# Performance work log

Measured on AMD Instinct MI355X. Metric: run time of the kernel, lower is better.

## Reference

```python
import jax, jax.numpy as jnp
import numpy as np
from jax import lax

GS = 29          # grid_size
DW = 15          # displacement_width
DR = 0.4         # disp_range
N = GS ** 3      # 24389 control points
P = DW ** 2      # 225 in-plane displacements
WIN = (1, 1, 3, 3, 1)
ONE = (1, 1, 1, 1, 1)


def _axis(n):
    # align_corners=False pixel-center coords in [-1, 1], as torch affine_grid
    return (2.0 * jnp.arange(n, dtype=jnp.float32) + 1.0) / n - 1.0


def make_grids():
    a = _axis(GS)
    zc, yc, xc = jnp.meshgrid(a, a, a, indexing='ij')
    grid_xyz = jnp.stack([xc, yc, zc], -1).reshape(-1, 3)  # (N,3) xyz, d-major flatten
    s = DR * _axis(DW)
    A, B = jnp.meshgrid(s, s, indexing='ij')
    Z = jnp.zeros_like(A)
    sx = jnp.stack([B, A, Z], -1).reshape(-1, 3)  # z=0 plane: (s[w], s[h], 0)
    sy = jnp.stack([B, Z, A], -1).reshape(-1, 3)  # y=0 plane: (s[w], 0, s[d])
    sz = jnp.stack([Z, B, A], -1).reshape(-1, 3)  # x=0 plane: (0, s[h], s[d])
    shift_2d = jnp.stack([sx, sy, sz], axis=1)    # (P,3,3): [disp, plane, xyz]
    return grid_xyz, shift_2d


def trilerp(vol, coords, border):
    # vol (C,D,H,W); coords (...,3) normalized xyz; align_corners=False trilinear
    C, D, H, W = vol.shape
    vflat = vol.reshape(C, -1)
    x, y, z = coords[..., 0], coords[..., 1], coords[..., 2]
    ix = 0.5 * ((x + 1.0) * W - 1.0)
    iy = 0.5 * ((y + 1.0) * H - 1.0)
    iz = 0.5 * ((z + 1.0) * D - 1.0)
    x0 = jnp.floor(ix); y0 = jnp.floor(iy); z0 = jnp.floor(iz)
    fx, fy, fz = ix - x0, iy - y0, iz - z0
    x0 = x0.astype(jnp.int32); y0 = y0.astype(jnp.int32); z0 = z0.astype(jnp.int32)
    out = 0.0
    for dz in (0, 1):
        wz = fz if dz else 1.0 - fz
        zi = z0 + dz
        for dy in (0, 1):
            wy = fy if dy else 1.0 - fy
            yi = y0 + dy
            for dx in (0, 1):
                wx = fx if dx else 1.0 - fx
                xi = x0 + dx
                w = wx * wy * wz
                xc = jnp.clip(xi, 0, W - 1)
                yc = jnp.clip(yi, 0, H - 1)
                zc = jnp.clip(zi, 0, D - 1)
                if not border:  # padding_mode='zeros'
                    inb = ((xi >= 0) & (xi < W) & (yi >= 0) & (yi < H) & (zi >= 0) & (zi < D))
                    w = w * inb.astype(vol.dtype)
                idx = (zc * H + yc) * W + xc
                out = out + vflat[:, idx] * w
    return out  # (C, *coords.shape[:-1])


def pad_dh(x):
    # ReplicationPad3d((0,0,2,2,2,2)) on a 5D tensor: pad dims 2 and 3 by 2
    return jnp.pad(x, ((0, 0), (0, 0), (2, 2), (2, 2), (0, 0)), mode='edge')


def minpool(x):
    # -MaxPool3d((3,3,1))(-x)
    return -lax.reduce_window(-x, -jnp.inf, lax.max, WIN, ONE, 'VALID')


def avgpool(x):
    # AvgPool3d((3,3,1), stride=1)
    return lax.reduce_window(x, 0.0, lax.add, WIN, ONE, 'VALID') / 9.0


def grid_smooth(cost):
    # (1,N,DW,DW,3) -> two 3x3 avg passes over the 29^3 control grid (d,h axes)
    cp = cost.transpose(2, 3, 4, 0, 1).reshape(1, 3 * P, GS, GS, GS)
    cp = avgpool(avgpool(pad_dh(cp)))
    return cp.transpose(0, 2, 3, 4, 1).reshape(1, N, DW, DW, 3)


def setup_inputs() -> dict:
    key = jax.random.key(0)
    k1, k2 = jax.random.split(key)
    C, V = 8, 64
    feat00 = jax.random.normal(k1, (1, C, V, V, V), jnp.float32)
    feat50 = jax.random.normal(k2, (1, C, V, V, V), jnp.float32)
    grid_xyz, shift_2d = make_grids()
    shift_2d_min = jnp.array(jnp.broadcast_to(shift_2d[None, None], (1, N, P, 3, 3)))
    alpha = jnp.array([1.0, 0.1, 1.0, 1.0, 0.1, 5.0], jnp.float32)
    return {"feat00": feat00, "feat50": feat50, "shift_2d_min": shift_2d_min,
            "grid_xyz": grid_xyz, "shift_2d": shift_2d, "alpha": alpha}


def reference(feat00, feat50, shift_2d_min, grid_xyz, shift_2d, alpha):
    grid29 = grid_xyz.reshape(GS, GS * GS, 3)
    sm = shift_2d_min.reshape(GS, GS * GS, P, 3, 3)
    f00, f50 = feat00[0], feat50[0]

    def chunk(args):
        g, s = args                                                # (841,3), (841,P,3,3)
        mov = trilerp(f50, g[:, None, None, :] + s, border=True)   # (C,841,P,3)
        fix = trilerp(f00, g, border=False)                        # (C,841)
        ssd = jnp.sum((fix[:, :, None, None] - mov) ** 2, axis=0)  # (841,P,3)
        return alpha[1] + alpha[0] * ssd

    pdd = lax.map(chunk, (grid29, sm)).reshape(1, N, DW, DW, 3)
    cost = avgpool(minpool(pad_dh(pdd)))
    cost = alpha[4] + alpha[2] * pdd + alpha[3] * grid_smooth(cost)
    cost = avgpool(minpool(pad_dh(cost)))
    cost_avg = grid_smooth(cost).reshape(N, P, 3)
    cost_soft = jax.nn.softmax(-alpha[5] * cost_avg, axis=1)
    pred_xyz = 0.5 * jnp.einsum('npk,pkd->nd', cost_soft, shift_2d)
    return cost_soft.reshape(N, 1, DW, DW, 3), pred_xyz, cost_avg
```

## Files before the change

### kernel.cpp

```cpp
#include <hip/hip_runtime.h>
#include <math.h>

#define GS   29
#define GS2  841
#define NCP  24389
#define DW   15
#define PP   225
#define CH   675
#define CHP  676
#define CC   8
#define VV   64
#define V3   262144

typedef __attribute__((ext_vector_type(8))) _Float16 half8;
typedef __attribute__((ext_vector_type(4))) _Float16 half4;

__device__ __forceinline__ float sv(int i) {
    return 0.4f * ((2.f * i + 1.f) * (1.f / 15.f) - 1.f);
}

__global__ __launch_bounds__(256) void make_vols(const float* __restrict__ in,
                                                 _Float16* __restrict__ volA,
                                                 _Float16* __restrict__ volB) {
    int v = blockIdx.x * 256 + threadIdx.x;
    if (v >= V3) return;
    int z = v >> 12, y = (v >> 6) & 63, x = v & 63;
    half8 h;
#pragma unroll
    for (int c = 0; c < CC; c++) h[c] = (_Float16)in[c * V3 + v];
    *(half8*)(volA + (size_t)v * 8) = h;
    *(half8*)(volB + (size_t)((((z << 6) | x) << 6) | y) * 8) = h;
}

__global__ __launch_bounds__(256) void pdd_pool_n(const float* __restrict__ f00,
                                                  const _Float16* __restrict__ volA,
                                                  const _Float16* __restrict__ volB,
                                                  const float* __restrict__ grid,
                                                  const float* __restrict__ alpha,
                                                  _Float16* __restrict__ pdd,
                                                  _Float16* __restrict__ pool) {
    int n = blockIdx.x;
    int tid = threadIdx.x;
    __shared__ __align__(16) _Float16 fixh[8];
    __shared__ float rowp[CH];
    __shared__ float smin[3 * 289];

    float gx = grid[n * 3 + 0], gy = grid[n * 3 + 1], gz = grid[n * 3 + 2];

    if (tid < 8) {
        float ix = 0.5f * ((gx + 1.f) * VV - 1.f);
        float iy = 0.5f * ((gy + 1.f) * VV - 1.f);
        float iz = 0.5f * ((gz + 1.f) * VV - 1.f);
        float x0f = floorf(ix), y0f = floorf(iy), z0f = floorf(iz);
        float fx = ix - x0f, fy = iy - y0f, fz = iz - z0f;
        int x0 = (int)x0f, y0 = (int)y0f, z0 = (int)z0f;
        const float* fc = f00 + tid * V3;
        float acc = 0.f;
        for (int dz = 0; dz < 2; dz++) {
            int zi = z0 + dz; float wz = dz ? fz : 1.f - fz;
            for (int dy = 0; dy < 2; dy++) {
                int yi = y0 + dy; float wy = dy ? fy : 1.f - fy;
                for (int dx = 0; dx < 2; dx++) {
                    int xi = x0 + dx; float wx = dx ? fx : 1.f - fx;
                    if (xi >= 0 && xi < VV && yi >= 0 && yi < VV && zi >= 0 && zi < VV)
                        acc += wx * wy * wz * fc[(zi * VV + yi) * VV + xi];
                }
            }
        }
        fixh[tid] = (_Float16)acc;
    }
    __syncthreads();

    if (tid < PP) {
        int p = tid;
        int h_ = p / 15, w_ = p - 15 * h_;
        float A = sv(h_), B = sv(w_);
        half8 f8 = *(const half8*)fixh;
        float a0 = alpha[0], a1 = alpha[1];

        for (int k = 0; k < 3; k++) {
            float pu, pv, pw;
            const _Float16* vol;
            if (k == 0)      { pu = gx + B; pv = gy + A; pw = gz;     vol = volA; }
            else if (k == 1) { pu = gx + B; pv = gy;     pw = gz + A; vol = volA; }
            else             { pu = gy + B; pv = gx;     pw = gz + A; vol = volB; }

            float iu = 0.5f * ((pu + 1.f) * VV - 1.f);
            float iv = 0.5f * ((pv + 1.f) * VV - 1.f);
            float iw = 0.5f * ((pw + 1.f) * VV - 1.f);
            float u0f = floorf(iu), v0f = floorf(iv), w0f = floorf(iw);
            float fu = iu - u0f, fv = iv - v0f, fw = iw - w0f;
            int u0 = (int)u0f, v0 = (int)v0f, w0 = (int)w0f;

            int p0 = min(max(u0, 0), VV - 2);
            float wAu = (u0 < 0) ? 1.f : ((u0 >= VV - 1) ? 0.f : (1.f - fu));
            float wBu = 1.f - wAu;
            int v0c = min(max(v0, 0), VV - 1), v1c = min(max(v0 + 1, 0), VV - 1);
            int w0c = min(max(w0, 0), VV - 1), w1c = min(max(w0 + 1, 0), VV - 1);
            float wv0 = 1.f - fv, wv1 = fv;
            float ww0 = 1.f - fw, ww1 = fw;

            half8 acc = {0, 0, 0, 0, 0, 0, 0, 0};
#define PAIR(WC, VC, WGT) {                                               \
                float fA_ = (WGT) * wAu, fB_ = (WGT) * wBu;               \
                _Float16 hA_ = (_Float16)fA_, hB_ = (_Float16)fB_;        \
                half8 hA8 = {hA_, hA_, hA_, hA_, hA_, hA_, hA_, hA_};     \
                half8 hB8 = {hB_, hB_, hB_, hB_, hB_, hB_, hB_, hB_};     \
                const _Float16* vp = vol + (size_t)((((WC) * VV) + (VC)) * VV + p0) * 8; \
                half8 lo = *(const half8*)vp;                             \
                half8 hi = *(const half8*)(vp + 8);                       \
                acc += hA8 * lo;                                          \
                acc += hB8 * hi;                                          \
            }
            PAIR(w0c, v0c, ww0 * wv0)
            PAIR(w0c, v1c, ww0 * wv1)
            PAIR(w1c, v0c, ww1 * wv0)
            PAIR(w1c, v1c, ww1 * wv1)
#undef PAIR

            half8 d8 = f8 - acc;
            float ssd = 0.f;
#pragma unroll
            for (int c = 0; c < 8; c++) { float dc = (float)d8[c]; ssd = fmaf(dc, dc, ssd); }
            rowp[p * 3 + k] = a1 + a0 * ssd;
        }
    }
    __syncthreads();

    for (int idx = tid; idx < 867; idx += 256) {
        int k = idx / 289; int r = idx - 289 * k; int a = r / 17; int b = r - 17 * a;
        float mn = 1e30f;
        for (int u = 0; u < 3; u++) {
            int hh = min(max(a + u - 2, 0), 14);
            for (int v = 0; v < 3; v++) {
                int ww = min(max(b + v - 2, 0), 14);
                mn = fminf(mn, rowp[(hh * 15 + ww) * 3 + k]);
            }
        }
        smin[idx] = mn;
    }
    __syncthreads();

    for (int i = tid; i < CH; i += 256) {
        pdd[(size_t)n * CHP + i] = (_Float16)rowp[i];
        int p = i / 3, k = i - 3 * p;
        int h = p / 15, w = p - 15 * h;
        float acc = 0.f;
        for (int a = 0; a < 3; a++)
            for (int b = 0; b < 3; b++)
                acc += smin[k * 289 + (h + a) * 17 + (w + b)];
        pool[(size_t)n * CHP + i] = (_Float16)(acc * (1.f / 9.f));
    }
}

__global__ __launch_bounds__(256) void gs_z4(const _Float16* __restrict__ in,
                                             _Float16* __restrict__ out) {
    const int COLS = GS2 * 169;
    int id = blockIdx.x * 256 + threadIdx.x;
    if (id >= COLS) return;
    int row = id / 169, c4 = id - 169 * row;
    size_t base = (size_t)row * CHP + c4 * 4;
    const size_t ZS = (size_t)GS2 * CHP;
    const float w0 = 1.f / 9.f, w1 = 2.f / 9.f, w2 = 3.f / 9.f;

    half4 h0 = *(const half4*)(in + base);
    half4 h3 = *(const half4*)(in + base + ZS);
    half4 h4 = *(const half4*)(in + base + 2 * ZS);
    float v0[4], v1[4], v2[4], v3[4], v4[4];
#pragma unroll
    for (int j = 0; j < 4; j++) {
        v0[j] = (float)h0[j]; v1[j] = v0[j]; v2[j] = v0[j];
        v3[j] = (float)h3[j]; v4[j] = (float)h4[j];
    }
    for (int z = 0; z < GS; z++) {
        half4 o;
#pragma unroll
        for (int j = 0; j < 4; j++)
            o[j] = (_Float16)(w0 * (v0[j] + v4[j]) + w1 * (v1[j] + v3[j]) + w2 * v2[j]);
        *(half4*)(out + base + (size_t)z * ZS) = o;
        int zn = z + 3; if (zn > GS - 1) zn = GS - 1;
        half4 hn = *(const half4*)(in + base + (size_t)zn * ZS);
#pragma unroll
        for (int j = 0; j < 4; j++) {
            v0[j] = v1[j]; v1[j] = v2[j]; v2[j] = v3[j]; v3[j] = v4[j];
            v4[j] = (float)hn[j];
        }
    }
}

__global__ __launch_bounds__(256) void cost_pool2_y(const _Float16* __restrict__ zs,
                                                    const _Float16* __restrict__ pdd,
                                                    const float* __restrict__ alpha,
                                                    _Float16* __restrict__ pool2) {
    int n = blockIdx.x, tid = threadIdx.x;
    int x = n % GS; int zy = n / GS; int y = zy % GS; int z = zy / GS;
    __shared__ float rowp[CHP];
    __shared__ float smn[17 * 17 * 3];

    if (tid < 169) {
        int c0 = tid * 4;
        float s0 = 0.f, s1 = 0.f, s2 = 0.f, s3 = 0.f;
#pragma unroll
        for (int dy = 0; dy < 5; dy++) {
            int yy = min(max(y + dy - 2, 0), GS - 1);
            size_t off = ((size_t)(z * GS + yy) * GS + x) * CHP + c0;
            float w = (3.f - fabsf((float)dy - 2.f)) * (1.f / 9.f);
            half4 hv = *(const half4*)(zs + off);
            s0 = fmaf(w, (float)hv[0], s0);
            s1 = fmaf(w, (float)hv[1], s1);
            s2 = fmaf(w, (float)hv[2], s2);
            s3 = fmaf(w, (float)hv[3], s3);
        }
        float a2 = alpha[2], a3 = alpha[3], a4 = alpha[4];
        half4 pv = *(const half4*)(pdd + (size_t)n * CHP + c0);
        rowp[c0 + 0] = a4 + a2 * (float)pv[0] + a3 * s0;
        rowp[c0 + 1] = a4 + a2 * (float)pv[1] + a3 * s1;
        rowp[c0 + 2] = a4 + a2 * (float)pv[2] + a3 * s2;
        rowp[c0 + 3] = a4 + a2 * (float)pv[3] + a3 * s3;
    }
    __syncthreads();

    for (int idx = tid; idx < 867; idx += 256) {
        int k = idx / 289; int r = idx - 289 * k; int a = r / 17; int b = r - 17 * a;
        float mn = 1e30f;
        for (int u = 0; u < 3; u++) {
            int hh = min(max(a + u - 2, 0), 14);
            for (int v = 0; v < 3; v++) {
                int ww = min(max(b + v - 2, 0), 14);
                mn = fminf(mn, rowp[(hh * 15 + ww) * 3 + k]);
            }
        }
        smn[idx] = mn;
    }
    __syncthreads();

    for (int i = tid; i < CH; i += 256) {
        int p = i / 3, k = i - 3 * p;
        int h = p / 15, w = p - 15 * h;
        float acc = 0.f;
        for (int a = 0; a < 3; a++)
            for (int b = 0; b < 3; b++)
                acc += smn[k * 289 + (h + a) * 17 + (w + b)];
        pool2[(size_t)n * CHP + i] = (_Float16)(acc * (1.f / 9.f));
    }
}

__global__ __launch_bounds__(256) void smooth_y_softmax(const _Float16* __restrict__ zs,
                                                        const float* __restrict__ alpha,
                                                        float* __restrict__ ca,
                                                        float* __restrict__ soft,
                                                        float* __restrict__ pred) {
    int n = blockIdx.x, tid = threadIdx.x;
    int x = n % GS; int zy = n / GS; int y = zy % GS; int z = zy / GS;
    int wave = tid >> 6, lane = tid & 63;
    __shared__ float vals[CHP];
    __shared__ float partial[3][3];

    if (tid < 169) {
        int c0 = tid * 4;
        float s0 = 0.f, s1 = 0.f, s2 = 0.f, s3 = 0.f;
#pragma unroll
        for (int dy = 0; dy < 5; dy++) {
            int yy = min(max(y + dy - 2, 0), GS - 1);
            size_t off = ((size_t)(z * GS + yy) * GS + x) * CHP + c0;
            float w = (3.f - fabsf((float)dy - 2.f)) * (1.f / 9.f);
            half4 hv = *(const half4*)(zs + off);
            s0 = fmaf(w, (float)hv[0], s0);
            s1 = fmaf(w, (float)hv[1], s1);
            s2 = fmaf(w, (float)hv[2], s2);
            s3 = fmaf(w, (float)hv[3], s3);
        }
        vals[c0 + 0] = s0;
        vals[c0 + 1] = s1;
        vals[c0 + 2] = s2;
        vals[c0 + 3] = s3;
    }
    __syncthreads();

    for (int i = tid; i < CH; i += 256) ca[(size_t)n * CH + i] = vals[i];
    __syncthreads();

    float a5 = alpha[5];
    if (wave < 3) {
        int k = wave;
        float v[4], e[4];
        float m = -1e30f;
#pragma unroll
        for (int j = 0; j < 4; j++) {
            int p = lane + 64 * j;
            v[j] = (p < PP) ? -a5 * vals[p * 3 + k] : -1e30f;
            m = fmaxf(m, v[j]);
        }
#pragma unroll
        for (int o = 32; o > 0; o >>= 1) m = fmaxf(m, __shfl_xor(m, o));
        float sum = 0.f;
#pragma unroll
        for (int j = 0; j < 4; j++) {
            int p = lane + 64 * j;
            e[j] = (p < PP) ? __expf(v[j] - m) : 0.f;
            sum += e[j];
        }
#pragma unroll
        for (int o = 32; o > 0; o >>= 1) sum += __shfl_xor(sum, o);
        float inv = 1.f / sum;
        float px = 0.f, py = 0.f, pz = 0.f;
#pragma unroll
        for (int j = 0; j < 4; j++) {
            int p = lane + 64 * j;
            if (p < PP) {
                float s = e[j] * inv;
                vals[p * 3 + k] = s;
                int h_ = p / 15, w_ = p - 15 * h_;
                float A = sv(h_), B = sv(w_);
                if (k == 0)      { px += s * B; py += s * A; }
                else if (k == 1) { px += s * B; pz += s * A; }
                else             { py += s * B; pz += s * A; }
            }
        }
#pragma unroll
        for (int o = 32; o > 0; o >>= 1) {
            px += __shfl_xor(px, o);
            py += __shfl_xor(py, o);
            pz += __shfl_xor(pz, o);
        }
        if (lane == 0) { partial[k][0] = px; partial[k][1] = py; partial[k][2] = pz; }
    }
    __syncthreads();
    if (tid < 3) pred[(size_t)n * 3 + tid] = 0.5f * (partial[0][tid] + partial[1][tid] + partial[2][tid]);
    for (int i = tid; i < CH; i += 256) soft[(size_t)n * CH + i] = vals[i];
}

extern "C" void kernel_launch(void* const* d_in, const int* in_sizes, int n_in,
                              void* d_out, int out_size, void* d_ws, size_t ws_size,
                              hipStream_t stream) {
    const float* f00   = (const float*)d_in[0];
    const float* f50   = (const float*)d_in[1];
    const float* grid  = (const float*)d_in[3];
    const float* alpha = (const float*)d_in[5];

    float* out0 = (float*)d_out;
    float* out1 = out0 + (size_t)NCP * CH;
    float* out2 = out1 + (size_t)NCP * 3;

    char* ws = (char*)d_ws;
    _Float16* volA = (_Float16*)ws;
    _Float16* volB = volA + (size_t)V3 * 8;
    _Float16* H0 = volB + (size_t)V3 * 8;
    _Float16* H1 = H0 + (size_t)NCP * CHP;
    _Float16* H2 = H1 + (size_t)NCP * CHP;

    make_vols<<<(V3 + 255) / 256, 256, 0, stream>>>(f50, volA, volB);

    pdd_pool_n<<<NCP, 256, 0, stream>>>(f00, volA, volB, grid, alpha, H0, H1);

    const int COLS = GS2 * 169;
    const int gbz = (COLS + 255) / 256;

    gs_z4<<<gbz, 256, 0, stream>>>(H1, H2);
    cost_pool2_y<<<NCP, 256, 0, stream>>>(H2, H0, alpha, H1);

    gs_z4<<<gbz, 256, 0, stream>>>(H1, H2);
    smooth_y_softmax<<<NCP, 256, 0, stream>>>(H2, alpha, out2, out0, out1);
}
```

Measured before the change: 534.2 us.

## Separate min/avg pooling into row/column passes and share per-axis trilinear setup

The 3x3 min-pool and 3x3 avg-pool are rewritten as separable passes, where each thread computes a strip of four outputs from six column reductions. This replaces nine scattered shared-memory reads per output with shared partial results. In the cost kernel, per-axis interpolation indices and weights are computed once and reused across the three planes, and the SSD reduction uses packed fp16 dot2. The pooled results are staged in shared memory so pdd and pool can be written as half4 vector stores, at the price of extra shared memory and a padding slot that must be zeroed.

After: 485.1 us. -9.2%, faster.

```diff
diff --git a/kernel.cpp b/kernel.cpp
--- a/kernel.cpp
+++ b/kernel.cpp
@@ -14,9 +14,67 @@
 
 typedef __attribute__((ext_vector_type(8))) _Float16 half8;
 typedef __attribute__((ext_vector_type(4))) _Float16 half4;
+typedef __attribute__((ext_vector_type(2))) _Float16 half2v;
 
 __device__ __forceinline__ float sv(int i) {
     return 0.4f * ((2.f * i + 1.f) * (1.f / 15.f) - 1.f);
+}
+
+__device__ __forceinline__ void paxis(float pc, int& p0, float& wA, float& wB) {
+    float iu = 0.5f * ((pc + 1.f) * (float)VV - 1.f);
+    float u0f = floorf(iu);
+    int u0 = (int)u0f;
+    p0 = min(max(u0, 0), VV - 2);
+    wA = (u0 < 0) ? 1.f : ((u0 >= VV - 1) ? 0.f : (1.f - (iu - u0f)));
+    wB = 1.f - wA;
+}
+__device__ __forceinline__ void vaxis(float pc, int& c0, int& c1, float& w0, float& w1) {
+    float iv = 0.5f * ((pc + 1.f) * (float)VV - 1.f);
+    float v0f = floorf(iv);
+    float fv = iv - v0f;
+    int v0 = (int)v0f;
+    c0 = min(max(v0, 0), VV - 1);
+    c1 = min(max(v0 + 1, 0), VV - 1);
+    w0 = 1.f - fv; w1 = fv;
+}
+
+__device__ __forceinline__ float sample_ssd(const _Float16* __restrict__ vol,
+        int p0, float wAu, float wBu,
+        int c0, int c1, float wv0, float wv1,
+        int e0, int e1, float ww0, float ww1,
+        half8 f8) {
+    half8 acc = {0, 0, 0, 0, 0, 0, 0, 0};
+#define PAIR(WC, VC, WGT) {                                               \
+        float fA_ = (WGT) * wAu, fB_ = (WGT) * wBu;                       \
+        _Float16 hA_ = (_Float16)fA_, hB_ = (_Float16)fB_;                \
+        half8 hA8 = {hA_, hA_, hA_, hA_, hA_, hA_, hA_, hA_};             \
+        half8 hB8 = {hB_, hB_, hB_, hB_, hB_, hB_, hB_, hB_};             \
+        const _Float16* vp = vol + (size_t)((((WC) * VV) + (VC)) * VV + p0) * 8; \
+        half8 lo = *(const half8*)vp;                                     \
+        half8 hi = *(const half8*)(vp + 8);                               \
+        acc += hA8 * lo;                                                  \
+        acc += hB8 * hi;                                                  \
+    }
+    PAIR(e0, c0, ww0 * wv0)
+    PAIR(e0, c1, ww0 * wv1)
+    PAIR(e1, c0, ww1 * wv0)
+    PAIR(e1, c1, ww1 * wv1)
+#undef PAIR
+    half8 d8 = f8 - acc;
+#if __has_builtin(__builtin_amdgcn_fdot2)
+    float ssd = 0.f;
+#pragma unroll
+    for (int j = 0; j < 4; j++) {
+        half2v d2 = {d8[2 * j], d8[2 * j + 1]};
+        ssd = __builtin_amdgcn_fdot2(d2, d2, ssd, false);
+    }
+    return ssd;
+#else
+    float ssd = 0.f;
+#pragma unroll
+    for (int c = 0; c < 8; c++) { float dc = (float)d8[c]; ssd = fmaf(dc, dc, ssd); }
+    return ssd;
+#endif
 }
 
 __global__ __launch_bounds__(256) void make_vols(const float* __restrict__ in,
@@ -42,11 +100,13 @@
     int n = blockIdx.x;
     int tid = threadIdx.x;
     __shared__ __align__(16) _Float16 fixh[8];
-    __shared__ float rowp[CH];
+    __shared__ float rowp[CHP];
     __shared__ float smin[3 * 289];
+    __shared__ float poolv[CHP];
 
     float gx = grid[n * 3 + 0], gy = grid[n * 3 + 1], gz = grid[n * 3 + 2];
 
+    if (tid == 8) { rowp[675] = 0.f; poolv[675] = 0.f; }
     if (tid < 8) {
         float ix = 0.5f * ((gx + 1.f) * VV - 1.f);
         float iy = 0.5f * ((gy + 1.f) * VV - 1.f);
@@ -78,78 +138,76 @@
         half8 f8 = *(const half8*)fixh;
         float a0 = alpha[0], a1 = alpha[1];
 
-        for (int k = 0; k < 3; k++) {
-            float pu, pv, pw;
-            const _Float16* vol;
-            if (k == 0)      { pu = gx + B; pv = gy + A; pw = gz;     vol = volA; }
-            else if (k == 1) { pu = gx + B; pv = gy;     pw = gz + A; vol = volA; }
-            else             { pu = gy + B; pv = gx;     pw = gz + A; vol = volB; }
-
-            float iu = 0.5f * ((pu + 1.f) * VV - 1.f);
-            float iv = 0.5f * ((pv + 1.f) * VV - 1.f);
-            float iw = 0.5f * ((pw + 1.f) * VV - 1.f);
-            float u0f = floorf(iu), v0f = floorf(iv), w0f = floorf(iw);
-            float fu = iu - u0f, fv = iv - v0f, fw = iw - w0f;
-            int u0 = (int)u0f, v0 = (int)v0f, w0 = (int)w0f;
-
-            int p0 = min(max(u0, 0), VV - 2);
-            float wAu = (u0 < 0) ? 1.f : ((u0 >= VV - 1) ? 0.f : (1.f - fu));
-            float wBu = 1.f - wAu;
-            int v0c = min(max(v0, 0), VV - 1), v1c = min(max(v0 + 1, 0), VV - 1);
-            int w0c = min(max(w0, 0), VV - 1), w1c = min(max(w0 + 1, 0), VV - 1);
-            float wv0 = 1.f - fv, wv1 = fv;
-            float ww0 = 1.f - fw, ww1 = fw;
-
-            half8 acc = {0, 0, 0, 0, 0, 0, 0, 0};
-#define PAIR(WC, VC, WGT) {                                               \
-                float fA_ = (WGT) * wAu, fB_ = (WGT) * wBu;               \
-                _Float16 hA_ = (_Float16)fA_, hB_ = (_Float16)fB_;        \
-                half8 hA8 = {hA_, hA_, hA_, hA_, hA_, hA_, hA_, hA_};     \
-                half8 hB8 = {hB_, hB_, hB_, hB_, hB_, hB_, hB_, hB_};     \
-                const _Float16* vp = vol + (size_t)((((WC) * VV) + (VC)) * VV + p0) * 8; \
-                half8 lo = *(const half8*)vp;                             \
-                half8 hi = *(const half8*)(vp + 8);                       \
-                acc += hA8 * lo;                                          \
-                acc += hB8 * hi;                                          \
-            }
-            PAIR(w0c, v0c, ww0 * wv0)
-            PAIR(w0c, v1c, ww0 * wv1)
-            PAIR(w1c, v0c, ww1 * wv0)
-            PAIR(w1c, v1c, ww1 * wv1)
-#undef PAIR
-
-            half8 d8 = f8 - acc;
-            float ssd = 0.f;
-#pragma unroll
-            for (int c = 0; c < 8; c++) { float dc = (float)d8[c]; ssd = fmaf(dc, dc, ssd); }
-            rowp[p * 3 + k] = a1 + a0 * ssd;
-        }
-    }
-    __syncthreads();
-
-    for (int idx = tid; idx < 867; idx += 256) {
-        int k = idx / 289; int r = idx - 289 * k; int a = r / 17; int b = r - 17 * a;
-        float mn = 1e30f;
-        for (int u = 0; u < 3; u++) {
-            int hh = min(max(a + u - 2, 0), 14);
-            for (int v = 0; v < 3; v++) {
-                int ww = min(max(b + v - 2, 0), 14);
-                mn = fminf(mn, rowp[(hh * 15 + ww) * 3 + k]);
-            }
-        }
-        smin[idx] = mn;
-    }
-    __syncthreads();
-
-    for (int i = tid; i < CH; i += 256) {
-        pdd[(size_t)n * CHP + i] = (_Float16)rowp[i];
-        int p = i / 3, k = i - 3 * p;
-        int h = p / 15, w = p - 15 * h;
-        float acc = 0.f;
-        for (int a = 0; a < 3; a++)
-            for (int b = 0; b < 3; b++)
-                acc += smin[k * 289 + (h + a) * 17 + (w + b)];
-        pool[(size_t)n * CHP + i] = (_Float16)(acc * (1.f / 9.f));
+        int pu01; float wAu01, wBu01; paxis(gx + B, pu01, wAu01, wBu01);
+        int pu2 ; float wAu2 , wBu2 ; paxis(gy + B, pu2 , wAu2 , wBu2 );
+        int va0, va1; float wva0, wva1; vaxis(gy + A, va0, va1, wva0, wva1);
+        int wa0, wa1; float wwa0, wwa1; vaxis(gz + A, wa0, wa1, wwa0, wwa1);
+        int zu0, zu1; float wzu0, wzu1; vaxis(gz, zu0, zu1, wzu0, wzu1);
+        int vy0, vy1; float wvy0, wvy1; vaxis(gy, vy0, vy1, wvy0, wvy1);
+        int vx0, vx1; float wvx0, wvx1; vaxis(gx, vx0, vx1, wvx0, wvx1);
+
+        float s0 = sample_ssd(volA, pu01, wAu01, wBu01, va0, va1, wva0, wva1, zu0, zu1, wzu0, wzu1, f8);
+        float s1 = sample_ssd(volA, pu01, wAu01, wBu01, vy0, vy1, wvy0, wvy1, wa0, wa1, wwa0, wwa1, f8);
+        float s2 = sample_ssd(volB, pu2 , wAu2 , wBu2 , vx0, vx1, wvx0, wvx1, wa0, wa1, wwa0, wwa1, f8);
+        rowp[p * 3 + 0] = a1 + a0 * s0;
+        rowp[p * 3 + 1] = a1 + a0 * s1;
+        rowp[p * 3 + 2] = a1 + a0 * s2;
+    }
+    __syncthreads();
+
+    if (tid < 255) {
+        int k = tid / 85, r = tid - 85 * k;
+        int a = r / 5, bc = r - 5 * a;
+        int b0 = bc * 4;
+        int ra = max(a - 2, 0) * 15;
+        int rb = min(max(a - 1, 0), 14) * 15;
+        int rc = min(a, 14) * 15;
+        float cm[6];
+#pragma unroll
+        for (int j = 0; j < 6; j++) {
+            int cj = min(max(b0 - 2 + j, 0), 14);
+            float m0 = rowp[(ra + cj) * 3 + k];
+            float m1 = rowp[(rb + cj) * 3 + k];
+            float m2 = rowp[(rc + cj) * 3 + k];
+            cm[j] = fminf(fminf(m0, m1), m2);
+        }
+#pragma unroll
+        for (int o = 0; o < 4; o++) {
+            int b = b0 + o;
+            if (b < 17) smin[k * 289 + a * 17 + b] = fminf(fminf(cm[o], cm[o + 1]), cm[o + 2]);
+        }
+    }
+    __syncthreads();
+
+    if (tid < 180) {
+        int k = tid / 60, r = tid - 60 * k;
+        int h = r >> 2, wc = r & 3;
+        int w0 = wc * 4;
+        const float* S = smin + k * 289;
+        float cs[6];
+#pragma unroll
+        for (int j = 0; j < 6; j++) {
+            int cj = min(w0 + j, 16);
+            cs[j] = S[h * 17 + cj] + S[(h + 1) * 17 + cj] + S[(h + 2) * 17 + cj];
+        }
+#pragma unroll
+        for (int o = 0; o < 4; o++) {
+            int w = w0 + o;
+            if (w < 15) poolv[(h * 15 + w) * 3 + k] = (cs[o] + cs[o + 1] + cs[o + 2]) * (1.f / 9.f);
+        }
+    }
+    __syncthreads();
+
+    if (tid < 169) {
+        int c0 = tid * 4;
+        half4 hp, hq;
+#pragma unroll
+        for (int j = 0; j < 4; j++) {
+            hp[j] = (_Float16)rowp[c0 + j];
+            hq[j] = (_Float16)poolv[c0 + j];
+        }
+        *(half4*)(pdd + (size_t)n * CHP + c0) = hp;
+        *(half4*)(pool + (size_t)n * CHP + c0) = hq;
     }
 }
 
@@ -195,8 +253,10 @@
     int n = blockIdx.x, tid = threadIdx.x;
     int x = n % GS; int zy = n / GS; int y = zy % GS; int z = zy / GS;
     __shared__ float rowp[CHP];
-    __shared__ float smn[17 * 17 * 3];
-
+    __shared__ float smin[3 * 289];
+    __shared__ float poolv[CHP];
+
+    if (tid == 169) poolv[675] = 0.f;
     if (tid < 169) {
         int c0 = tid * 4;
         float s0 = 0.f, s1 = 0.f, s2 = 0.f, s3 = 0.f;
@@ -220,28 +280,55 @@
     }
     __syncthreads();
 
-    for (int idx = tid; idx < 867; idx += 256) {
-        int k = idx / 289; int r = idx - 289 * k; int a = r / 17; int b = r - 17 * a;
-        float mn = 1e30f;
-        for (int u = 0; u < 3; u++) {
-            int hh = min(max(a + u - 2, 0), 14);
-            for (int v = 0; v < 3; v++) {
-                int ww = min(max(b + v - 2, 0), 14);
-                mn = fminf(mn, rowp[(hh * 15 + ww) * 3 + k]);
-            }
-        }
-        smn[idx] = mn;
-    }
-    __syncthreads();
-
-    for (int i = tid; i < CH; i += 256) {
-        int p = i / 3, k = i - 3 * p;
-        int h = p / 15, w = p - 15 * h;
-        float acc = 0.f;
-        for (int a = 0; a < 3; a++)
-            for (int b = 0; b < 3; b++)
-                acc += smn[k * 289 + (h + a) * 17 + (w + b)];
-        pool2[(size_t)n * CHP + i] = (_Float16)(acc * (1.f / 9.f));
+    if (tid < 255) {
+        int k = tid / 85, r = tid - 85 * k;
+        int a = r / 5, bc = r - 5 * a;
+        int b0 = bc * 4;
+        int ra = max(a - 2, 0) * 15;
+        int rb = min(max(a - 1, 0), 14) * 15;
+        int rc = min(a, 14) * 15;
+        float cm[6];
+#pragma unroll
+        for (int j = 0; j < 6; j++) {
+            int cj = min(max(b0 - 2 + j, 0), 14);
+            float m0 = rowp[(ra + cj) * 3 + k];
+            float m1 = rowp[(rb + cj) * 3 + k];
+            float m2 = rowp[(rc + cj) * 3 + k];
+            cm[j] = fminf(fminf(m0, m1), m2);
+        }
+#pragma unroll
+        for (int o = 0; o < 4; o++) {
+            int b = b0 + o;
+            if (b < 17) smin[k * 289 + a * 17 + b] = fminf(fminf(cm[o], cm[o + 1]), cm[o + 2]);
+        }
+    }
+    __syncthreads();
+
+    if (tid < 180) {
+        int k = tid / 60, r = tid - 60 * k;
+        int h = r >> 2, wc = r & 3;
+        int w0 = wc * 4;
+        const float* S = smin + k * 289;
+        float cs[6];
+#pragma unroll
+        for (int j = 0; j < 6; j++) {
+            int cj = min(w0 + j, 16);
+            cs[j] = S[h * 17 + cj] + S[(h + 1) * 17 + cj] + S[(h + 2) * 17 + cj];
+        }
+#pragma unroll
+        for (int o = 0; o < 4; o++) {
+            int w = w0 + o;
+            if (w < 15) poolv[(h * 15 + w) * 3 + k] = (cs[o] + cs[o + 1] + cs[o + 2]) * (1.f / 9.f);
+        }
+    }
+    __syncthreads();
+
+    if (tid < 169) {
+        int c0 = tid * 4;
+        half4 hq;
+#pragma unroll
+        for (int j = 0; j < 4; j++) hq[j] = (_Float16)poolv[c0 + j];
+        *(half4*)(pool2 + (size_t)n * CHP + c0) = hq;
     }
 }
 
```
